# Kernel optimization log

Hardware: AMD Instinct MI355X
Metric: run time of the kernel (lower is better)

The kernel has to match this reference:

```python
import jax, jax.numpy as jnp
import numpy as np

N, L, S, H, D = 1, 4096, 4096, 8, 32


def setup_inputs() -> dict:
    key = jax.random.key(0)
    k1, k2, k3 = jax.random.split(key, 3)
    q = jax.random.normal(k1, (N, L, H, D), dtype=jnp.float32)
    k = jax.random.normal(k2, (N, S, H, D), dtype=jnp.float32)
    v = jax.random.normal(k3, (N, S, H, D), dtype=jnp.float32)
    q_mask = jnp.ones((N, L), dtype=bool)
    kv_mask = jnp.ones((N, S), dtype=bool)
    return {"q": q, "k": k, "v": v, "q_mask": q_mask, "kv_mask": kv_mask}


def reference(q, k, v, q_mask, kv_mask):
    # qk: [N, L, S, H] -- full score tensor as in the torch module
    qk = jnp.einsum('nlhd,nshd->nlsh', q, k)
    # mask BEFORE scaling (matches torch: masked_fill then divide by sqrt(D))
    mask = ~(q_mask[:, :, None, None] & kv_mask[:, None, :, None])
    qk = jnp.where(mask, jnp.float32(-1e9), qk)
    scale = q.shape[3] ** 0.5
    attn = jax.nn.softmax(qk / scale, axis=2)  # softmax over S
    out = jnp.einsum('nlsh,nshd->nlhd', attn, v)
    return out
```

## Files before the change

kernel.cpp:

```cpp
#include <hip/hip_runtime.h>
#include <hip/hip_bf16.h>

typedef __bf16 bf16x4 __attribute__((ext_vector_type(4)));
typedef __bf16 bf16x8 __attribute__((ext_vector_type(8)));
typedef float  f32x4  __attribute__((ext_vector_type(4)));

#define H_  8
#define D_  32
#define L_  4096
#define S_  4096
#define BM  64
#define BN  64
#define NSPLIT 4

static __device__ __forceinline__ f32x4 mfma_k16(bf16x4 a, bf16x4 b, f32x4 c) {
#if __has_builtin(__builtin_amdgcn_mfma_f32_16x16x16_bf16)
    return __builtin_amdgcn_mfma_f32_16x16x16_bf16(a, b, c, 0, 0, 0);
#elif __has_builtin(__builtin_amdgcn_mfma_f32_16x16x16bf16_1k)
    typedef short s16x4 __attribute__((ext_vector_type(4)));
    union U { bf16x4 h; s16x4 s; };
    U ua, ub; ua.h = a; ub.h = b;
    return __builtin_amdgcn_mfma_f32_16x16x16bf16_1k(ua.s, ub.s, c, 0, 0, 0);
#else
    asm("v_mfma_f32_16x16x16_bf16 %0, %1, %2, %0" : "+v"(c) : "v"(a), "v"(b));
    return c;
#endif
}

__global__ __launch_bounds__(256)
void prep_k(const float* __restrict__ kk, __bf16* __restrict__ kb)
{
    const int oi = blockIdx.x * 256 + threadIdx.x;
    const int h    = oi >> 14;
    const int s    = (oi >> 2) & (S_ - 1);
    const int dseg = (oi & 3) * 8;
    const float* ip = kk + (((size_t)s * H_ + h) * D_ + dseg);
    float4 a = *(const float4*)ip, b = *(const float4*)(ip + 4);
    bf16x8 o;
    o[0]=(__bf16)a.x; o[1]=(__bf16)a.y; o[2]=(__bf16)a.z; o[3]=(__bf16)a.w;
    o[4]=(__bf16)b.x; o[5]=(__bf16)b.y; o[6]=(__bf16)b.z; o[7]=(__bf16)b.w;
    *(bf16x8*)(kb + ((size_t)h * S_ + s) * D_ + dseg) = o;
}

__global__ __launch_bounds__(256)
void prep_v(const float* __restrict__ v, __bf16* __restrict__ vt)
{
    const int h  = blockIdx.y;
    const int s0 = blockIdx.x * 64;
    __shared__ __bf16 T[D_][72];
    const int sr = threadIdx.x >> 2, dseg = (threadIdx.x & 3) * 8;
    const float* ip = v + (((size_t)(s0 + sr) * H_ + h) * D_ + dseg);
    float4 a = *(const float4*)ip, b = *(const float4*)(ip + 4);
    float vv[8] = {a.x, a.y, a.z, a.w, b.x, b.y, b.z, b.w};
#pragma unroll
    for (int j = 0; j < 8; ++j) T[dseg + j][sr] = (__bf16)vv[j];
    __syncthreads();
    const int d = threadIdx.x >> 3, so = (threadIdx.x & 7) * 8;
    bf16x8 o = *(const bf16x8*)(&T[d][so]);
    *(bf16x8*)(vt + ((size_t)h * D_ + d) * S_ + s0 + so) = o;
}

__global__ __launch_bounds__(256, 6)
void fattn_v2(const __bf16* __restrict__ kb, const __bf16* __restrict__ vtg,
              const float* __restrict__ q, float* __restrict__ num,
              float* __restrict__ den, int schunk)
{
    const int qt = blockIdx.x, h = blockIdx.y, sp = blockIdx.z;
    const int tid = threadIdx.x, wave = tid >> 6, lane = tid & 63;
    const int col = lane & 15, quad = lane >> 4;

    __shared__ __align__(16) __bf16 Ks[2][BN][40];
    __shared__ __align__(16) __bf16 Vt[2][D_][72];

    const float cs = 0.17677669529663687f * 1.4426950408889634f;

    const int qn = qt * BM + wave * 16 + col;
    bf16x8 qb;
    {
        const float* qp = q + ((size_t)qn * H_ + h) * D_ + quad * 8;
        float4 q0 = *(const float4*)qp;
        float4 q1 = *(const float4*)(qp + 4);
        qb[0]=(__bf16)(q0.x*cs); qb[1]=(__bf16)(q0.y*cs);
        qb[2]=(__bf16)(q0.z*cs); qb[3]=(__bf16)(q0.w*cs);
        qb[4]=(__bf16)(q1.x*cs); qb[5]=(__bf16)(q1.y*cs);
        qb[6]=(__bf16)(q1.z*cs); qb[7]=(__bf16)(q1.w*cs);
    }

    f32x4 o0 = {0,0,0,0}, o1 = {0,0,0,0}, accl = {0,0,0,0};
    const f32x4 zc = {0,0,0,0};
    const bf16x4 ones = {(__bf16)1.f, (__bf16)1.f, (__bf16)1.f, (__bf16)1.f};

    const int srow = tid >> 2, kseg = (tid & 3) * 8;
    const int vd   = tid >> 3, vso  = (tid & 7) * 8;
    const int vcolw = (vso + 16 * (vd >> 3)) & 63;
    const int rot0  = (col >> 3) << 4;

    const int sbeg = sp * schunk;
    const int T = schunk / BN;

    const __bf16* kptr = kb  + ((size_t)h * S_ + sbeg + srow) * D_ + kseg;
    const __bf16* vptr = vtg + ((size_t)h * D_ + vd) * S_ + sbeg + vso;

    bf16x8 kf = *(const bf16x8*)kptr;
    bf16x8 vf = *(const bf16x8*)vptr;
    bf16x8 kn = kf, vn = vf;

    for (int t = 0; t < T; ++t) {
        const int b = t & 1;
        *(bf16x8*)(&Ks[b][srow][kseg]) = kf;
        *(bf16x8*)(&Vt[b][vd][vcolw])  = vf;
        if (t + 1 < T) {
            kn = *(const bf16x8*)(kptr + (size_t)(t + 1) * BN * D_);
            vn = *(const bf16x8*)(vptr + (t + 1) * BN);
        }
        __syncthreads();

#pragma unroll
        for (int sb = 0; sb < 4; ++sb) {
            bf16x8 ka = *(const bf16x8*)(&Ks[b][sb * 16 + col][quad * 8]);
            f32x4 st = __builtin_amdgcn_mfma_f32_16x16x32_bf16(ka, qb, zc, 0, 0, 0);
            bf16x4 pb;
#pragma unroll
            for (int r = 0; r < 4; ++r)
                pb[r] = (__bf16)__builtin_amdgcn_exp2f(st[r]);
            const int sc  = sb * 16 + quad * 4;
            bf16x4 va0 = *(const bf16x4*)(&Vt[b][col     ][(sc + rot0)      & 63]);
            bf16x4 va1 = *(const bf16x4*)(&Vt[b][col + 16][(sc + rot0 + 32) & 63]);
            o0   = mfma_k16(va0,  pb, o0);
            o1   = mfma_k16(va1,  pb, o1);
            accl = mfma_k16(ones, pb, accl);
        }
        kf = kn; vf = vn;
    }

    float* pr = num + (((size_t)(sp * H_ + h) * L_ + qn) << 5);
    *(f32x4*)(pr + quad * 4)      = o0;
    *(f32x4*)(pr + 16 + quad * 4) = o1;
    if (quad == 0) den[(size_t)(sp * H_ + h) * L_ + qn] = accl[0];
}

template<bool DIRECT>
__global__ __launch_bounds__(256, 6)
void fattn_main(const float* __restrict__ q, const float* __restrict__ kk,
                const float* __restrict__ v, float* __restrict__ num,
                float* __restrict__ den, float* __restrict__ out, int schunk)
{
    const int qt = blockIdx.x, h = blockIdx.y, sp = blockIdx.z;
    const int tid = threadIdx.x, wave = tid >> 6, lane = tid & 63;
    const int col = lane & 15, quad = lane >> 4;

    __shared__ __align__(16) __bf16 Ks[2][BN][40];
    __shared__ __align__(16) __bf16 Vt[2][D_][72];

    const float cs = 0.17677669529663687f * 1.4426950408889634f;

    const int qn = qt * BM + wave * 16 + col;
    bf16x8 qb;
    {
        const float* qp = q + ((size_t)qn * H_ + h) * D_ + quad * 8;
        float4 q0 = *(const float4*)qp;
        float4 q1 = *(const float4*)(qp + 4);
        qb[0]=(__bf16)(q0.x*cs); qb[1]=(__bf16)(q0.y*cs);
        qb[2]=(__bf16)(q0.z*cs); qb[3]=(__bf16)(q0.w*cs);
        qb[4]=(__bf16)(q1.x*cs); qb[5]=(__bf16)(q1.y*cs);
        qb[6]=(__bf16)(q1.z*cs); qb[7]=(__bf16)(q1.w*cs);
    }

    f32x4 o0 = {0,0,0,0}, o1 = {0,0,0,0}, accl = {0,0,0,0};
    const f32x4 zc = {0,0,0,0};
    const bf16x4 ones = {(__bf16)1.f, (__bf16)1.f, (__bf16)1.f, (__bf16)1.f};

    const int srow = tid >> 2;
    const int g    = tid & 3;
    const int dseg = g * 8;
    const int vcol = (srow + 16 * g) & 63;
    const int rot0 = (col >> 3) << 4;

    const int sbeg = sp * schunk;
    const int T = schunk / BN;

    float4 kf0, kf1, vf0, vf1;
    {
        const size_t goff = ((size_t)(sbeg + srow) * H_ + h) * D_ + dseg;
        kf0 = *(const float4*)(kk + goff);
        kf1 = *(const float4*)(kk + goff + 4);
        vf0 = *(const float4*)(v + goff);
        vf1 = *(const float4*)(v + goff + 4);
    }
    float4 kn0 = kf0, kn1 = kf1, vn0 = vf0, vn1 = vf1;

    for (int t = 0; t < T; ++t) {
        const int b = t & 1;
        {
            bf16x8 kb;
            kb[0]=(__bf16)kf0.x; kb[1]=(__bf16)kf0.y; kb[2]=(__bf16)kf0.z; kb[3]=(__bf16)kf0.w;
            kb[4]=(__bf16)kf1.x; kb[5]=(__bf16)kf1.y; kb[6]=(__bf16)kf1.z; kb[7]=(__bf16)kf1.w;
            *(bf16x8*)(&Ks[b][srow][dseg]) = kb;
            float vv[8] = {vf0.x, vf0.y, vf0.z, vf0.w, vf1.x, vf1.y, vf1.z, vf1.w};
#pragma unroll
            for (int j = 0; j < 8; ++j)
                Vt[b][dseg + j][vcol] = (__bf16)vv[j];
        }
        if (t + 1 < T) {
            const size_t goff = ((size_t)(sbeg + (t+1)*BN + srow) * H_ + h) * D_ + dseg;
            kn0 = *(const float4*)(kk + goff);
            kn1 = *(const float4*)(kk + goff + 4);
            vn0 = *(const float4*)(v + goff);
            vn1 = *(const float4*)(v + goff + 4);
        }
        __syncthreads();

#pragma unroll
        for (int sb = 0; sb < 4; ++sb) {
            bf16x8 ka = *(const bf16x8*)(&Ks[b][sb * 16 + col][quad * 8]);
            f32x4 st = __builtin_amdgcn_mfma_f32_16x16x32_bf16(ka, qb, zc, 0, 0, 0);
            bf16x4 pb;
#pragma unroll
            for (int r = 0; r < 4; ++r)
                pb[r] = (__bf16)__builtin_amdgcn_exp2f(st[r]);
            const int sc  = sb * 16 + quad * 4;
            bf16x4 va0 = *(const bf16x4*)(&Vt[b][col     ][(sc + rot0)      & 63]);
            bf16x4 va1 = *(const bf16x4*)(&Vt[b][col + 16][(sc + rot0 + 32) & 63]);
            o0   = mfma_k16(va0,  pb, o0);
            o1   = mfma_k16(va1,  pb, o1);
            accl = mfma_k16(ones, pb, accl);
        }
        kf0 = kn0; kf1 = kn1; vf0 = vn0; vf1 = vn1;
    }

    if (DIRECT) {
        const float inv = 1.f / accl[0];
        float* op = out + ((size_t)qn * H_ + h) * D_;
        f32x4 r0 = {o0[0]*inv, o0[1]*inv, o0[2]*inv, o0[3]*inv};
        f32x4 r1 = {o1[0]*inv, o1[1]*inv, o1[2]*inv, o1[3]*inv};
        *(f32x4*)(op + quad * 4)      = r0;
        *(f32x4*)(op + 16 + quad * 4) = r1;
    } else {
        float* pr = num + (((size_t)(sp * H_ + h) * L_ + qn) << 5);
        *(f32x4*)(pr + quad * 4)      = o0;
        *(f32x4*)(pr + 16 + quad * 4) = o1;
        if (quad == 0) den[(size_t)(sp * H_ + h) * L_ + qn] = accl[0];
    }
}

__global__ __launch_bounds__(256)
void fattn_combine(const float* __restrict__ num, const float* __restrict__ den,
                   float* __restrict__ out)
{
    const int i  = blockIdx.x * 256 + threadIdx.x;
    const int d4 = (i & 7) * 4;
    const int h  = (i >> 3) & 7;
    const int l  = i >> 6;
    f32x4 acc = {0,0,0,0};
    float dn = 0.f;
    for (int sp = 0; sp < NSPLIT; ++sp) {
        const float* pr = num + (((size_t)(sp * H_ + h) * L_ + l) << 5) + d4;
        f32x4 t = *(const f32x4*)pr;
        acc[0] += t[0]; acc[1] += t[1]; acc[2] += t[2]; acc[3] += t[3];
        dn += den[(size_t)(sp * H_ + h) * L_ + l];
    }
    const float inv = 1.f / dn;
    f32x4 r = {acc[0]*inv, acc[1]*inv, acc[2]*inv, acc[3]*inv};
    *(f32x4*)(out + ((size_t)l * H_ + h) * D_ + d4) = r;
}

extern "C" void kernel_launch(void* const* d_in, const int* in_sizes, int n_in,
                              void* d_out, int out_size, void* d_ws, size_t ws_size,
                              hipStream_t stream) {
    const float* q = (const float*)d_in[0];
    const float* k = (const float*)d_in[1];
    const float* v = (const float*)d_in[2];
    float* out = (float*)d_out;
    const size_t nnum = (size_t)NSPLIT * H_ * L_ * 32;
    const size_t nden = (size_t)NSPLIT * H_ * L_;
    const size_t nkv  = (size_t)H_ * S_ * D_;
    const size_t need_v2 = (nnum + nden) * sizeof(float) + 2 * nkv * sizeof(__bf16);
    if (ws_size >= need_v2) {
        float* num = (float*)d_ws;
        float* den = num + nnum;
        __bf16* kbp = (__bf16*)(den + nden);
        __bf16* vtp = kbp + nkv;
        prep_k<<<dim3((H_ * S_ * D_ / 8) / 256), 256, 0, stream>>>(k, kbp);
        prep_v<<<dim3(S_ / 64, H_), 256, 0, stream>>>(v, vtp);
        fattn_v2<<<dim3(L_ / BM, H_, NSPLIT), 256, 0, stream>>>(
            kbp, vtp, q, num, den, S_ / NSPLIT);
        fattn_combine<<<dim3((L_ * H_ * D_ / 4) / 256), 256, 0, stream>>>(num, den, out);
    } else if (ws_size >= (nnum + nden) * sizeof(float)) {
        float* num = (float*)d_ws;
        float* den = num + nnum;
        fattn_main<false><<<dim3(L_ / BM, H_, NSPLIT), 256, 0, stream>>>(
            q, k, v, num, den, out, S_ / NSPLIT);
        fattn_combine<<<dim3((L_ * H_ * D_ / 4) / 256), 256, 0, stream>>>(num, den, out);
    } else {
        fattn_main<true><<<dim3(L_ / BM, H_, 1), 256, 0, stream>>>(
            q, k, v, nullptr, nullptr, out, S_);
    }
}
```

Measured before the change: 112.2 us.

## Switch attention core to 32x32x16 MFMA with 128-query tiles

Replaces the 16x16 MFMA attention kernel with one that uses 32x32x16 bf16 MFMAs, so each wave handles 32 queries and each block 128 queries. P is packed to bf16 with v_cvt_pk and redistributed across half-waves with v_permlane32_swap, and the softmax denominator is now summed with VALU adds instead of a ones-vector MFMA. The aim is fewer, larger matrix instructions and better K/V reuse per block. In exchange it raises register pressure (occupancy hint drops to 4), halves the grid size, and relies on gfx950-specific instructions.

```diff
diff --git a/kernel.cpp b/kernel.cpp
--- a/kernel.cpp
+++ b/kernel.cpp
@@ -4,23 +4,20 @@
 typedef __bf16 bf16x4 __attribute__((ext_vector_type(4)));
 typedef __bf16 bf16x8 __attribute__((ext_vector_type(8)));
 typedef float  f32x4  __attribute__((ext_vector_type(4)));
+typedef float  f32x16 __attribute__((ext_vector_type(16)));
 
 #define H_  8
 #define D_  32
 #define L_  4096
 #define S_  4096
 #define BM  64
+#define BM4 128
 #define BN  64
 #define NSPLIT 4
 
 static __device__ __forceinline__ f32x4 mfma_k16(bf16x4 a, bf16x4 b, f32x4 c) {
 #if __has_builtin(__builtin_amdgcn_mfma_f32_16x16x16_bf16)
     return __builtin_amdgcn_mfma_f32_16x16x16_bf16(a, b, c, 0, 0, 0);
-#elif __has_builtin(__builtin_amdgcn_mfma_f32_16x16x16bf16_1k)
-    typedef short s16x4 __attribute__((ext_vector_type(4)));
-    union U { bf16x4 h; s16x4 s; };
-    U ua, ub; ua.h = a; ub.h = b;
-    return __builtin_amdgcn_mfma_f32_16x16x16bf16_1k(ua.s, ub.s, c, 0, 0, 0);
 #else
     asm("v_mfma_f32_16x16x16_bf16 %0, %1, %2, %0" : "+v"(c) : "v"(a), "v"(b));
     return c;
@@ -60,40 +57,42 @@
     *(bf16x8*)(vt + ((size_t)h * D_ + d) * S_ + s0 + so) = o;
 }
 
-__global__ __launch_bounds__(256, 6)
-void fattn_v2(const __bf16* __restrict__ kb, const __bf16* __restrict__ vtg,
+__global__ __launch_bounds__(256, 4)
+void fattn_v4(const __bf16* __restrict__ kb, const __bf16* __restrict__ vtg,
               const float* __restrict__ q, float* __restrict__ num,
               float* __restrict__ den, int schunk)
 {
     const int qt = blockIdx.x, h = blockIdx.y, sp = blockIdx.z;
-    const int tid = threadIdx.x, wave = tid >> 6, lane = tid & 63;
-    const int col = lane & 15, quad = lane >> 4;
-
-    __shared__ __align__(16) __bf16 Ks[2][BN][40];
+    const int tid = threadIdx.x, wq = tid >> 6, lane = tid & 63;
+    const int ln = lane & 31, hl = lane >> 5;
+
+    __shared__ __align__(16) __bf16 Ks[2][64][40];
     __shared__ __align__(16) __bf16 Vt[2][D_][72];
 
     const float cs = 0.17677669529663687f * 1.4426950408889634f;
 
-    const int qn = qt * BM + wave * 16 + col;
-    bf16x8 qb;
+    const int qn = qt * BM4 + wq * 32 + ln;
+    bf16x8 qf0, qf1;
     {
-        const float* qp = q + ((size_t)qn * H_ + h) * D_ + quad * 8;
-        float4 q0 = *(const float4*)qp;
-        float4 q1 = *(const float4*)(qp + 4);
-        qb[0]=(__bf16)(q0.x*cs); qb[1]=(__bf16)(q0.y*cs);
-        qb[2]=(__bf16)(q0.z*cs); qb[3]=(__bf16)(q0.w*cs);
-        qb[4]=(__bf16)(q1.x*cs); qb[5]=(__bf16)(q1.y*cs);
-        qb[6]=(__bf16)(q1.z*cs); qb[7]=(__bf16)(q1.w*cs);
-    }
-
-    f32x4 o0 = {0,0,0,0}, o1 = {0,0,0,0}, accl = {0,0,0,0};
-    const f32x4 zc = {0,0,0,0};
-    const bf16x4 ones = {(__bf16)1.f, (__bf16)1.f, (__bf16)1.f, (__bf16)1.f};
+        const float* qp = q + ((size_t)qn * H_ + h) * D_ + hl * 8;
+        float4 a = *(const float4*)qp,        b = *(const float4*)(qp + 4);
+        float4 c = *(const float4*)(qp + 16), d = *(const float4*)(qp + 20);
+        qf0[0]=(__bf16)(a.x*cs); qf0[1]=(__bf16)(a.y*cs);
+        qf0[2]=(__bf16)(a.z*cs); qf0[3]=(__bf16)(a.w*cs);
+        qf0[4]=(__bf16)(b.x*cs); qf0[5]=(__bf16)(b.y*cs);
+        qf0[6]=(__bf16)(b.z*cs); qf0[7]=(__bf16)(b.w*cs);
+        qf1[0]=(__bf16)(c.x*cs); qf1[1]=(__bf16)(c.y*cs);
+        qf1[2]=(__bf16)(c.z*cs); qf1[3]=(__bf16)(c.w*cs);
+        qf1[4]=(__bf16)(d.x*cs); qf1[5]=(__bf16)(d.y*cs);
+        qf1[6]=(__bf16)(d.z*cs); qf1[7]=(__bf16)(d.w*cs);
+    }
+
+    f32x16 o = {0,0,0,0,0,0,0,0,0,0,0,0,0,0,0,0};
+    const f32x16 z16 = {0,0,0,0,0,0,0,0,0,0,0,0,0,0,0,0};
+    f32x4 accl = {0,0,0,0};
 
     const int srow = tid >> 2, kseg = (tid & 3) * 8;
     const int vd   = tid >> 3, vso  = (tid & 7) * 8;
-    const int vcolw = (vso + 16 * (vd >> 3)) & 63;
-    const int rot0  = (col >> 3) << 4;
 
     const int sbeg = sp * schunk;
     const int T = schunk / BN;
@@ -108,7 +107,7 @@
     for (int t = 0; t < T; ++t) {
         const int b = t & 1;
         *(bf16x8*)(&Ks[b][srow][kseg]) = kf;
-        *(bf16x8*)(&Vt[b][vd][vcolw])  = vf;
+        *(bf16x8*)(&Vt[b][vd][vso])    = vf;
         if (t + 1 < T) {
             kn = *(const bf16x8*)(kptr + (size_t)(t + 1) * BN * D_);
             vn = *(const bf16x8*)(vptr + (t + 1) * BN);
@@ -116,27 +115,50 @@
         __syncthreads();
 
 #pragma unroll
-        for (int sb = 0; sb < 4; ++sb) {
-            bf16x8 ka = *(const bf16x8*)(&Ks[b][sb * 16 + col][quad * 8]);
-            f32x4 st = __builtin_amdgcn_mfma_f32_16x16x32_bf16(ka, qb, zc, 0, 0, 0);
-            bf16x4 pb;
-#pragma unroll
-            for (int r = 0; r < 4; ++r)
-                pb[r] = (__bf16)__builtin_amdgcn_exp2f(st[r]);
-            const int sc  = sb * 16 + quad * 4;
-            bf16x4 va0 = *(const bf16x4*)(&Vt[b][col     ][(sc + rot0)      & 63]);
-            bf16x4 va1 = *(const bf16x4*)(&Vt[b][col + 16][(sc + rot0 + 32) & 63]);
-            o0   = mfma_k16(va0,  pb, o0);
-            o1   = mfma_k16(va1,  pb, o1);
-            accl = mfma_k16(ones, pb, accl);
+        for (int sh = 0; sh < 2; ++sh) {
+            bf16x8 ka0 = *(const bf16x8*)(&Ks[b][sh * 32 + ln][hl * 8]);
+            bf16x8 ka1 = *(const bf16x8*)(&Ks[b][sh * 32 + ln][16 + hl * 8]);
+            f32x16 st = __builtin_amdgcn_mfma_f32_32x32x16_bf16(ka0, qf0, z16, 0, 0, 0);
+            st = __builtin_amdgcn_mfma_f32_32x32x16_bf16(ka1, qf1, st, 0, 0, 0);
+            float p[16];
+#pragma unroll
+            for (int r = 0; r < 16; ++r) p[r] = __builtin_amdgcn_exp2f(st[r]);
+            accl[0] += p[0]  + p[1]  + p[2]  + p[3];
+            accl[1] += p[4]  + p[5]  + p[6]  + p[7];
+            accl[2] += p[8]  + p[9]  + p[10] + p[11];
+            accl[3] += p[12] + p[13] + p[14] + p[15];
+#pragma unroll
+            for (int u = 0; u < 2; ++u) {
+                unsigned A, B, C, D;
+                asm("v_cvt_pk_bf16_f32 %0, %1, %2" : "=v"(A) : "v"(p[u*8+0]), "v"(p[u*8+1]));
+                asm("v_cvt_pk_bf16_f32 %0, %1, %2" : "=v"(B) : "v"(p[u*8+2]), "v"(p[u*8+3]));
+                asm("v_cvt_pk_bf16_f32 %0, %1, %2" : "=v"(C) : "v"(p[u*8+4]), "v"(p[u*8+5]));
+                asm("v_cvt_pk_bf16_f32 %0, %1, %2" : "=v"(D) : "v"(p[u*8+6]), "v"(p[u*8+7]));
+                asm("v_permlane32_swap_b32 %0, %1" : "+v"(A), "+v"(C));
+                asm("v_permlane32_swap_b32 %0, %1" : "+v"(B), "+v"(D));
+                union { unsigned w[4]; bf16x8 f; } pb;
+                pb.w[0] = A; pb.w[1] = B; pb.w[2] = C; pb.w[3] = D;
+                const int slot = sh * 2 + u;
+                bf16x8 va = *(const bf16x8*)(&Vt[b][ln][slot * 16 + hl * 8]);
+                o = __builtin_amdgcn_mfma_f32_32x32x16_bf16(va, pb.f, o, 0, 0, 0);
+            }
         }
         kf = kn; vf = vn;
     }
 
+    float dsum = accl[0] + accl[1] + accl[2] + accl[3];
+    dsum += __shfl_xor(dsum, 32, 64);
+
     float* pr = num + (((size_t)(sp * H_ + h) * L_ + qn) << 5);
-    *(f32x4*)(pr + quad * 4)      = o0;
-    *(f32x4*)(pr + 16 + quad * 4) = o1;
-    if (quad == 0) den[(size_t)(sp * H_ + h) * L_ + qn] = accl[0];
+    f32x4 w0 = {o[0],  o[1],  o[2],  o[3]};
+    f32x4 w1 = {o[4],  o[5],  o[6],  o[7]};
+    f32x4 w2 = {o[8],  o[9],  o[10], o[11]};
+    f32x4 w3 = {o[12], o[13], o[14], o[15]};
+    *(f32x4*)(pr      + hl * 4) = w0;
+    *(f32x4*)(pr + 8  + hl * 4) = w1;
+    *(f32x4*)(pr + 16 + hl * 4) = w2;
+    *(f32x4*)(pr + 24 + hl * 4) = w3;
+    if (hl == 0) den[(size_t)(sp * H_ + h) * L_ + qn] = dsum;
 }
 
 template<bool DIRECT>
@@ -274,15 +296,15 @@
     const size_t nnum = (size_t)NSPLIT * H_ * L_ * 32;
     const size_t nden = (size_t)NSPLIT * H_ * L_;
     const size_t nkv  = (size_t)H_ * S_ * D_;
-    const size_t need_v2 = (nnum + nden) * sizeof(float) + 2 * nkv * sizeof(__bf16);
-    if (ws_size >= need_v2) {
+    const size_t need_v4 = (nnum + nden) * sizeof(float) + 2 * nkv * sizeof(__bf16);
+    if (ws_size >= need_v4) {
         float* num = (float*)d_ws;
         float* den = num + nnum;
         __bf16* kbp = (__bf16*)(den + nden);
         __bf16* vtp = kbp + nkv;
         prep_k<<<dim3((H_ * S_ * D_ / 8) / 256), 256, 0, stream>>>(k, kbp);
         prep_v<<<dim3(S_ / 64, H_), 256, 0, stream>>>(v, vtp);
-        fattn_v2<<<dim3(L_ / BM, H_, NSPLIT), 256, 0, stream>>>(
+        fattn_v4<<<dim3(L_ / BM4, H_, NSPLIT), 256, 0, stream>>>(
             kbp, vtp, q, num, den, S_ / NSPLIT);
         fattn_combine<<<dim3((L_ * H_ * D_ / 4) / 256), 256, 0, stream>>>(num, den, out);
     } else if (ws_size >= (nnum + nden) * sizeof(float)) {
```

New measurement: 105.4 us. 1.06x faster.
